# Performance work log

Hardware: AMD Instinct MI355X
Metric: run time of the kernel (lower is better)

## Reference

```python
import jax, jax.numpy as jnp
import numpy as np

B, T, E, H, HD = 4, 1500, 1280, 20, 64
SCALING = HD ** -0.5


def setup_inputs() -> dict:
    key = jax.random.key(0)
    ks = jax.random.split(key, 8)
    s = 0.02
    return {
        "hidden_states": jax.random.normal(ks[0], (B, 1, T, E), jnp.float32),
        "attention_mask": jnp.zeros((B, 1, T, T), jnp.float32),
        "Wq": jax.random.normal(ks[1], (H, HD, E), jnp.float32) * s,
        "bq": jax.random.normal(ks[2], (H, HD), jnp.float32) * s,
        "Wk": jax.random.normal(ks[3], (H, HD, E), jnp.float32) * s,
        "Wv": jax.random.normal(ks[4], (H, HD, E), jnp.float32) * s,
        "bv": jax.random.normal(ks[5], (H, HD), jnp.float32) * s,
        "Wo": jax.random.normal(ks[6], (E, E), jnp.float32) * s,
        "bo": jax.random.normal(ks[7], (E,), jnp.float32) * s,
    }


def reference(hidden_states, attention_mask, Wq, bq, Wk, Wv, bv, Wo, bo):
    # hidden_states: [B, 1, T, E] (NHWC with H=1, as in the torch module)
    b, _, t, e = hidden_states.shape
    x = hidden_states[:, 0]  # [B, T, E]
    # Per-head 1x1 Conv2d projections == batched linear over stacked head weights.
    # Scaling is folded into q (the module bakes it into q_proj weights/bias).
    q = (jnp.einsum("bte,hde->bhtd", x, Wq) + bq[None, :, None, :]) * SCALING
    k = jnp.einsum("bse,hde->bhsd", x, Wk)
    v = jnp.einsum("bse,hde->bhsd", x, Wv) + bv[None, :, None, :]
    # attention_mask broadcasts over the head dim (module adds it per head as [B,1,T,S])
    scores = jnp.einsum("bhtd,bhsd->bhts", q, k) + attention_mask  # [B,H,T,S]
    attn = jax.nn.softmax(scores, axis=-1)
    out = jnp.einsum("bhts,bhsd->bhtd", attn, v)  # [B,H,T,HD]
    out = out.transpose(0, 2, 1, 3).reshape(b, t, e)  # concat heads on channel dim
    final = jnp.einsum("bte,fe->btf", out, Wo) + bo  # 1x1 Conv2d out_proj
    return final[:, None, :, :]  # [B,1,T,E]
```

## Files before the change

kernel.cpp:

```cpp
#include <hip/hip_runtime.h>

#define T_LEN 1500
#define TP    1536
#define EDIM  1280
#define NH    20
#define HD    64
#define KDIM  1280
#define NT    20

#define LOG2E 1.4426950408889634f

#define OFF_X    ((size_t)0)
#define OFF_AO   ((size_t)0)
#define OFF_W    ((size_t)7700480)
#define OFF_WO   ((size_t)12615680)
#define OFF_Q    ((size_t)14254080)
#define OFF_K    ((size_t)22118400)
#define OFF_VT   ((size_t)29982720)

typedef float  f32x4  __attribute__((ext_vector_type(4)));
typedef float  f32x16 __attribute__((ext_vector_type(16)));
typedef short  s16x8  __attribute__((ext_vector_type(8)));
typedef __bf16 bf16x8 __attribute__((ext_vector_type(8)));
typedef unsigned short u16;
typedef unsigned int   u32;
typedef unsigned int u32x4 __attribute__((ext_vector_type(4)));

__device__ __forceinline__ f32x4 mfma_bf16(s16x8 a, s16x8 b, f32x4 c) {
  return __builtin_amdgcn_mfma_f32_16x16x32_bf16(
      __builtin_bit_cast(bf16x8, a), __builtin_bit_cast(bf16x8, b), c, 0, 0, 0);
}

__device__ __forceinline__ f32x16 mfma32(s16x8 a, s16x8 b, f32x16 c) {
  return __builtin_amdgcn_mfma_f32_32x32x16_bf16(
      __builtin_bit_cast(bf16x8, a), __builtin_bit_cast(bf16x8, b), c, 0, 0, 0);
}

__device__ __forceinline__ u16 f2bf(float f) {
  union { float f; unsigned int u; } a; a.f = f;
  return (u16)((a.u + 0x7fffu + ((a.u >> 16) & 1u)) >> 16);
}

__device__ __forceinline__ float fexp2(float x) {
  return __builtin_amdgcn_exp2f(x);
}

__device__ __forceinline__ void gl_lds16(const u16* g, u16* l) {
  __builtin_amdgcn_global_load_lds(
      (const __attribute__((address_space(1))) unsigned int*)(const void*)g,
      (__attribute__((address_space(3))) unsigned int*)(void*)l, 16, 0, 0);
}


__global__ __launch_bounds__(256) void prep_kernel(
    const float* __restrict__ x, const float* __restrict__ wq,
    const float* __restrict__ wk, const float* __restrict__ wv,
    const float* __restrict__ wo, const float* __restrict__ mask,
    u16* __restrict__ ws, u32* __restrict__ nzflags) {
  const int S0 = 1925120;
  const int S1 = 1228800;
  const int S2 = 409600;
  const int P1 = 46080;
  const int S3 = 2250000;
  const int TOT = S0 + S1 + S2 + 3 * P1 + S3;
  for (int v = blockIdx.x * 256 + threadIdx.x; v < TOT; v += gridDim.x * 256) {
    if (v < S0) {
      int i = v * 4;
      int m = i / EDIM, e = i - m * EDIM;
      int ep = (e & ~63) | (((((e >> 3) & 7) ^ (m & 7))) << 3) | (e & 7);
      ushort4 o;
      if (m < 6000) {
        float4 f = *(const float4*)(x + i);
        o = make_ushort4(f2bf(f.x), f2bf(f.y), f2bf(f.z), f2bf(f.w));
      } else {
        o = make_ushort4(0, 0, 0, 0);
      }
      *(ushort4*)(ws + OFF_X + (size_t)m * EDIM + ep) = o;
    } else if (v < S0 + S1) {
      int j = (v - S0) * 4;
      int n = j / EDIM, e = j - n * EDIM;
      const float* s = (n < 1280) ? wq + (size_t)n * EDIM + e
                     : (n < 2560) ? wk + (size_t)(n - 1280) * EDIM + e
                                  : wv + (size_t)(n - 2560) * EDIM + e;
      float4 f = *(const float4*)s;
      int ep = (e & ~63) | (((((e >> 3) & 7) ^ (n & 7))) << 3) | (e & 7);
      *(ushort4*)(ws + OFF_W + (size_t)n * EDIM + ep) =
          make_ushort4(f2bf(f.x), f2bf(f.y), f2bf(f.z), f2bf(f.w));
    } else if (v < S0 + S1 + S2) {
      int j = (v - S0 - S1) * 4;
      int n = j / EDIM, e = j - n * EDIM;
      float4 f = *(const float4*)(wo + j);
      int ep = (e & ~63) | (((((e >> 3) & 7) ^ (n & 7))) << 3) | (e & 7);
      *(ushort4*)(ws + OFF_WO + (size_t)n * EDIM + ep) =
          make_ushort4(f2bf(f.x), f2bf(f.y), f2bf(f.z), f2bf(f.w));
    } else if (v < S0 + S1 + S2 + 3 * P1) {
      int p = v - (S0 + S1 + S2);
      ushort4 z = make_ushort4(0, 0, 0, 0);
      if (p < P1) {
        int p4 = p * 4; int bh = p4 / 2304; int rem = p4 - bh * 2304;
        int tt = rem >> 6, d = rem & 63;
        *(ushort4*)(ws + OFF_Q + ((size_t)(bh * TP + 1500 + tt)) * HD + d) = z;
      } else if (p < 2 * P1) {
        int p4 = (p - P1) * 4; int bh = p4 / 2304; int rem = p4 - bh * 2304;
        int tt = rem >> 6, d = rem & 63;
        *(ushort4*)(ws + OFF_K + ((size_t)(bh * TP + 1500 + tt)) * HD + d) = z;
      } else {
        int p4 = (p - 2 * P1) * 4; int bh = p4 / 2304; int rem = p4 - bh * 2304;
        int d = rem / 36, ss = rem - d * 36;
        int t = 1500 + ss;
        int tphys = (t & ~63) | (((((t >> 3) & 7) ^ (d & 7))) << 3) | (t & 7);
        *(ushort4*)(ws + OFF_VT + ((size_t)(bh * HD + d)) * TP + tphys) = z;
      }
    } else {
      int p = v - (S0 + S1 + S2 + 3 * P1);
      int i4 = p * 4;
      int bb = i4 / 2250000;
      int rem = i4 - bb * 2250000;
      int q = rem / 1500;
      int s = rem - q * 1500;
      float4 f = *(const float4*)(mask + (size_t)bb * 2250000 + rem);
      if (f.x != 0.f || f.y != 0.f || f.z != 0.f || f.w != 0.f)
        atomicOr(&nzflags[(bb * 12 + (q >> 7)) * 24 + (s >> 6)], 1u);
    }
  }
}

__device__ __forceinline__ void gemm_mainloop256(
    const u16* __restrict__ A, const u16* __restrict__ B,
    int mt, int nt, u16* lds, f32x4 acc[4][4]) {
  const int tid = threadIdx.x;
  const int lane = tid & 63, wid = tid >> 6;
  const int lg = lane >> 4, lr = lane & 15;
  const int wr = wid >> 1, wn = wid & 1;

  const u16* aB = A + (size_t)(mt * 256) * KDIM;
  const u16* bB = B + (size_t)(nt * 128) * KDIM;
  size_t aOff[4], bOff[2];
  #pragma unroll
  for (int l = 0; l < 4; ++l) {
    int gid = l * 512 + tid;
    aOff[l] = (size_t)(gid >> 3) * KDIM + (gid & 7) * 8;
  }
  #pragma unroll
  for (int l = 0; l < 2; ++l) {
    int gid = l * 512 + tid;
    bOff[l] = (size_t)(gid >> 3) * KDIM + (gid & 7) * 8;
  }
  const int ldsOff = tid * 8;
  int arow[4], brow[4];
  #pragma unroll
  for (int i = 0; i < 4; ++i) arow[i] = (wr * 64 + i * 16 + lr) * 64;
  #pragma unroll
  for (int j = 0; j < 4; ++j) brow[j] = (wn * 64 + j * 16 + lr) * 64;
  const int gsw0 = ((lg) ^ (lr & 7)) * 8;
  const int gsw1 = ((4 + lg) ^ (lr & 7)) * 8;

  #pragma unroll
  for (int t = 0; t < 2; ++t) {
    u16* dA = lds + t * 24576;
    u16* dB = dA + 16384;
    #pragma unroll
    for (int l = 0; l < 4; ++l) gl_lds16(aB + aOff[l] + t * 64, dA + ldsOff + l * 4096);
    #pragma unroll
    for (int l = 0; l < 2; ++l) gl_lds16(bB + bOff[l] + t * 64, dB + ldsOff + l * 4096);
  }

  int s = 0;
  #pragma unroll 1
  for (int kt = 0; kt < NT; ++kt) {
    if (kt < NT - 1) asm volatile("s_waitcnt vmcnt(6)" ::: "memory");
    else             asm volatile("s_waitcnt vmcnt(0)" ::: "memory");
    __builtin_amdgcn_s_barrier();
    __builtin_amdgcn_sched_barrier(0);
    u16* cA = lds + s * 24576;
    u16* cB = cA + 16384;
    int ssl = s + 2; if (ssl >= 3) ssl -= 3;
    u16* sA = lds + ssl * 24576;
    u16* sB = sA + 16384;
    const bool doStage = (kt + 2 < NT);
    if (doStage) {
      gl_lds16(aB + aOff[0] + (kt + 2) * 64, sA + ldsOff);
      gl_lds16(aB + aOff[1] + (kt + 2) * 64, sA + ldsOff + 4096);
      gl_lds16(bB + bOff[0] + (kt + 2) * 64, sB + ldsOff);
    }
    {
      s16x8 af[4], bg[4];
      #pragma unroll
      for (int i = 0; i < 4; ++i) af[i] = *(const s16x8*)(cA + arow[i] + gsw0);
      #pragma unroll
      for (int j = 0; j < 4; ++j) bg[j] = *(const s16x8*)(cB + brow[j] + gsw0);
      __builtin_amdgcn_s_setprio(1);
      #pragma unroll
      for (int i = 0; i < 4; ++i)
        #pragma unroll
        for (int j = 0; j < 4; ++j)
          acc[i][j] = mfma_bf16(af[i], bg[j], acc[i][j]);
      __builtin_amdgcn_s_setprio(0);
    }
    __builtin_amdgcn_s_barrier();
    if (doStage) {
      gl_lds16(aB + aOff[2] + (kt + 2) * 64, sA + ldsOff + 8192);
      gl_lds16(aB + aOff[3] + (kt + 2) * 64, sA + ldsOff + 12288);
      gl_lds16(bB + bOff[1] + (kt + 2) * 64, sB + ldsOff + 4096);
    }
    {
      s16x8 af[4], bg[4];
      #pragma unroll
      for (int i = 0; i < 4; ++i) af[i] = *(const s16x8*)(cA + arow[i] + gsw1);
      #pragma unroll
      for (int j = 0; j < 4; ++j) bg[j] = *(const s16x8*)(cB + brow[j] + gsw1);
      __builtin_amdgcn_s_setprio(1);
      #pragma unroll
      for (int i = 0; i < 4; ++i)
        #pragma unroll
        for (int j = 0; j < 4; ++j)
          acc[i][j] = mfma_bf16(af[i], bg[j], acc[i][j]);
      __builtin_amdgcn_s_setprio(0);
    }
    s = s + 1; if (s >= 3) s = 0;
  }
}

__global__ __launch_bounds__(512) void gemm_qkv_kernel(
    const u16* __restrict__ X, const u16* __restrict__ W,
    const float* __restrict__ bq, const float* __restrict__ bv,
    u16* __restrict__ Qw, u16* __restrict__ Kw, u16* __restrict__ Vtw) {
  __shared__ __align__(16) u16 lds[3 * 24576];
  const int bid = blockIdx.x;
  const int xcd = bid & 7, idx = bid >> 3;
  const int mt = xcd * 3 + idx % 3;
  const int nt = idx / 3;
  f32x4 acc[4][4] = {};
  gemm_mainloop256(X, W, mt, nt, lds, acc);
  const int tid = threadIdx.x;
  const int lane = tid & 63, wid = tid >> 6;
  const int lg = lane >> 4, lr = lane & 15;
  const int wr = wid >> 1, wn = wid & 1;
  #pragma unroll
  for (int i = 0; i < 4; ++i) {
    #pragma unroll
    for (int r = 0; r < 4; ++r) {
      int mm = mt * 256 + wr * 64 + i * 16 + lg * 4 + r;
      if (mm >= 6000) continue;
      int bt = mm / 1500, tt = mm - bt * 1500;
      #pragma unroll
      for (int j = 0; j < 4; ++j) {
        int n = nt * 128 + wn * 64 + j * 16 + lr;
        float v = acc[i][j][r];
        if (n < 1280) {
          int hh = n >> 6, d = n & 63;
          Qw[((size_t)(bt * NH + hh) * TP + tt) * HD + d] =
              f2bf((v + bq[n]) * (0.125f * LOG2E));
        } else if (n < 2560) {
          int nn = n - 1280, hh = nn >> 6, d = nn & 63;
          int dp = ((((d >> 3) ^ (tt & 7))) << 3) | (d & 7);
          Kw[((size_t)(bt * NH + hh) * TP + tt) * HD + dp] = f2bf(v);
        } else {
          int nn = n - 2560, hh = nn >> 6, d = nn & 63;
          int tphys = (tt & ~63) | (((((tt >> 3) & 7) ^ (d & 7))) << 3) | (tt & 7);
          Vtw[((size_t)(bt * NH + hh) * HD + d) * TP + tphys] = f2bf(v + bv[nn]);
        }
      }
    }
  }
}

__global__ __launch_bounds__(256) void attn_kernel(
    const u16* __restrict__ Qw, const u16* __restrict__ Kw,
    const u16* __restrict__ Vtw, const float* __restrict__ mask,
    const u32* __restrict__ nzflags, u16* __restrict__ AO) {
  __shared__ __align__(16) u16 Kb[2][64 * 64];
  __shared__ __align__(16) u16 Vb[2][64 * 64];
  const int bhid = blockIdx.y;
  const int bb = bhid / NH, hh = bhid % NH;
  const int tid = threadIdx.x;
  const int w = tid >> 6;
  const int lane = tid & 63;
  const int lq = lane & 31;
  const int hi = lane >> 5;
  const int q0 = blockIdx.x * 128 + w * 32;
  const int qrow = q0 + lq;
  const int qm = qrow < (T_LEN - 1) ? qrow : (T_LEN - 1);
  const u16* Qp = Qw + (size_t)bhid * TP * HD;
  const u16* Kp = Kw + (size_t)bhid * TP * HD;
  const u16* Vp = Vtw + (size_t)bhid * HD * TP;
  const float* mp = mask + (size_t)bb * T_LEN * T_LEN + (size_t)qm * T_LEN;
  const u32* nzp = nzflags + (bb * 12 + blockIdx.x) * 24;

  s16x8 qf[4];
  #pragma unroll
  for (int c = 0; c < 4; ++c)
    qf[c] = *(const s16x8*)(Qp + (size_t)qrow * HD + c * 16 + hi * 8);

  f32x16 O0 = {}, O1 = {};
  float m = -3e38f, l = 0.f;

  {
    gl_lds16(Kp + tid * 8,                 Kb[0] + tid * 8);
    gl_lds16(Kp + 2048 + tid * 8,          Kb[0] + 2048 + tid * 8);
    int r = tid >> 3, g = tid & 7;
    gl_lds16(Vp + (size_t)r * TP + g * 8,          Vb[0] + tid * 8);
    gl_lds16(Vp + (size_t)(r + 32) * TP + g * 8,   Vb[0] + 2048 + tid * 8);
  }
  __syncthreads();

  int buf = 0;
  #pragma unroll 1
  for (int st = 0; st < 24; ++st) {
    const int s0 = st * 64;
    if (st < 23) {
      const int sn = s0 + 64;
      gl_lds16(Kp + (size_t)sn * HD + tid * 8,        Kb[buf ^ 1] + tid * 8);
      gl_lds16(Kp + (size_t)sn * HD + 2048 + tid * 8, Kb[buf ^ 1] + 2048 + tid * 8);
      int r = tid >> 3, g = tid & 7;
      gl_lds16(Vp + (size_t)r * TP + sn + g * 8,        Vb[buf ^ 1] + tid * 8);
      gl_lds16(Vp + (size_t)(r + 32) * TP + sn + g * 8, Vb[buf ^ 1] + 2048 + tid * 8);
    }
    const bool has_mask = nzp[st] != 0u;
    const u16* kb = Kb[buf];
    f32x16 S0a = {}, S1a = {};
    #pragma unroll
    for (int c = 0; c < 4; ++c) {
      int gc = 2 * c + hi;
      int gs = (gc ^ (lq & 7)) << 3;
      s16x8 k0 = *(const s16x8*)(kb + lq * 64 + gs);
      s16x8 k1 = *(const s16x8*)(kb + (32 + lq) * 64 + gs);
      S0a = mfma32(k0, qf[c], S0a);
      S1a = mfma32(k1, qf[c], S1a);
    }
    float p[32];
    #pragma unroll
    for (int r = 0; r < 16; ++r) { p[r] = S0a[r]; p[16 + r] = S1a[r]; }
    if (has_mask) {
      f32x4 mk[2][4];
      #pragma unroll
      for (int sh = 0; sh < 2; ++sh)
        #pragma unroll
        for (int g = 0; g < 4; ++g) {
          int sb = s0 + sh * 32 + 8 * g + 4 * hi;
          if (sb > T_LEN - 4) sb = T_LEN - 4;
          mk[sh][g] = *(const f32x4*)(mp + sb);
        }
      #pragma unroll
      for (int r = 0; r < 16; ++r) {
        p[r]      = fmaf(mk[0][r >> 2][r & 3], LOG2E, p[r]);
        p[16 + r] = fmaf(mk[1][r >> 2][r & 3], LOG2E, p[16 + r]);
      }
    }
    if (st == 23) {
      if (hi) { p[12] = p[13] = p[14] = p[15] = -1e30f; }
      #pragma unroll
      for (int r = 16; r < 32; ++r) p[r] = -1e30f;
    }
    float t1[16];
    #pragma unroll
    for (int r = 0; r < 16; ++r) t1[r] = fmaxf(p[r], p[r + 16]);
    #pragma unroll
    for (int r = 0; r < 8; ++r) t1[r] = fmaxf(t1[r], t1[r + 8]);
    float mx = fmaxf(fmaxf(fmaxf(t1[0], t1[1]), fmaxf(t1[2], t1[3])),
                     fmaxf(fmaxf(t1[4], t1[5]), fmaxf(t1[6], t1[7])));
    mx = fmaxf(mx, __shfl_xor(mx, 32));
    if (!__all(mx <= m + 8.f)) {
      float mn = fmaxf(m, mx);
      float sc = fexp2(m - mn);
      O0 *= sc; O1 *= sc; l *= sc;
      m = mn;
    }
    #pragma unroll
    for (int r = 0; r < 32; ++r) p[r] = fexp2(p[r] - m);
    float s1[16];
    #pragma unroll
    for (int r = 0; r < 16; ++r) s1[r] = p[r] + p[r + 16];
    #pragma unroll
    for (int r = 0; r < 8; ++r) s1[r] += s1[r + 8];
    #pragma unroll
    for (int r = 0; r < 4; ++r) s1[r] += s1[r + 4];
    float rs = (s1[0] + s1[1]) + (s1[2] + s1[3]);
    rs += __shfl_xor(rs, 32);
    l += rs;
    const u16* vb = Vb[buf];
    #pragma unroll
    for (int sh = 0; sh < 2; ++sh) {
      u32 pk[8];
      #pragma unroll
      for (int j = 0; j < 8; ++j)
        asm("v_cvt_pk_bf16_f32 %0, %1, %2"
            : "=v"(pk[j]) : "v"(p[sh * 16 + 2 * j]), "v"(p[sh * 16 + 2 * j + 1]));
      asm("v_permlane32_swap_b32 %0, %1" : "+v"(pk[0]), "+v"(pk[2]));
      asm("v_permlane32_swap_b32 %0, %1" : "+v"(pk[1]), "+v"(pk[3]));
      asm("v_permlane32_swap_b32 %0, %1" : "+v"(pk[4]), "+v"(pk[6]));
      asm("v_permlane32_swap_b32 %0, %1" : "+v"(pk[5]), "+v"(pk[7]));
      u32x4 ta = {pk[0], pk[1], pk[2], pk[3]};
      u32x4 tb = {pk[4], pk[5], pk[6], pk[7]};
      s16x8 pfa = __builtin_bit_cast(s16x8, ta);
      s16x8 pfb = __builtin_bit_cast(s16x8, tb);
      int ga = sh * 4 + hi, gb = sh * 4 + 2 + hi;
      {
        int d = lq;
        s16x8 va = *(const s16x8*)(vb + d * 64 + ((ga ^ (d & 7)) << 3));
        s16x8 vc = *(const s16x8*)(vb + d * 64 + ((gb ^ (d & 7)) << 3));
        O0 = mfma32(va, pfa, O0);
        O0 = mfma32(vc, pfb, O0);
      }
      {
        int d = 32 + lq;
        s16x8 va = *(const s16x8*)(vb + d * 64 + ((ga ^ (d & 7)) << 3));
        s16x8 vc = *(const s16x8*)(vb + d * 64 + ((gb ^ (d & 7)) << 3));
        O1 = mfma32(va, pfa, O1);
        O1 = mfma32(vc, pfb, O1);
      }
    }
    __syncthreads();
    buf ^= 1;
  }

  if (qrow < T_LEN) {
    float inv = 1.f / l;
    int arow = bb * T_LEN + qrow;
    int key = arow & 7;
    size_t base = (size_t)arow * EDIM + hh * 64;
    #pragma unroll
    for (int g = 0; g < 4; ++g) {
      ushort4 o0, o1;
      o0.x = f2bf(O0[4 * g + 0] * inv); o0.y = f2bf(O0[4 * g + 1] * inv);
      o0.z = f2bf(O0[4 * g + 2] * inv); o0.w = f2bf(O0[4 * g + 3] * inv);
      o1.x = f2bf(O1[4 * g + 0] * inv); o1.y = f2bf(O1[4 * g + 1] * inv);
      o1.z = f2bf(O1[4 * g + 2] * inv); o1.w = f2bf(O1[4 * g + 3] * inv);
      *(ushort4*)(AO + base + ((g ^ key) << 3) + 4 * hi)       = o0;
      *(ushort4*)(AO + base + (((4 + g) ^ key) << 3) + 4 * hi) = o1;
    }
  }
}

__global__ __launch_bounds__(512) void gemm_out_kernel(
    const u16* __restrict__ AOb, const u16* __restrict__ Wob,
    const float* __restrict__ bo, float* __restrict__ out) {
  __shared__ __align__(16) u16 lds[3 * 24576];
  const int bid = blockIdx.x;
  const int xcd = bid & 7, idx = bid >> 3;
  const int mt = xcd * 3 + idx % 3;
  const int nt = idx / 3;
  f32x4 acc[4][4] = {};
  gemm_mainloop256(AOb, Wob, mt, nt, lds, acc);
  const int tid = threadIdx.x;
  const int lane = tid & 63, wid = tid >> 6;
  const int lg = lane >> 4, lr = lane & 15;
  const int wr = wid >> 1, wn = wid & 1;
  #pragma unroll
  for (int i = 0; i < 4; ++i) {
    #pragma unroll
    for (int r = 0; r < 4; ++r) {
      int mm = mt * 256 + wr * 64 + i * 16 + lg * 4 + r;
      if (mm >= 6000) continue;
      #pragma unroll
      for (int j = 0; j < 4; ++j) {
        int n = nt * 128 + wn * 64 + j * 16 + lr;
        out[(size_t)mm * EDIM + n] = acc[i][j][r] + bo[n];
      }
    }
  }
}

extern "C" void kernel_launch(void* const* d_in, const int* in_sizes, int n_in,
                              void* d_out, int out_size, void* d_ws, size_t ws_size,
                              hipStream_t stream) {
  const float* x    = (const float*)d_in[0];
  const float* mask = (const float*)d_in[1];
  const float* wq   = (const float*)d_in[2];
  const float* bq   = (const float*)d_in[3];
  const float* wk   = (const float*)d_in[4];
  const float* wv   = (const float*)d_in[5];
  const float* bv   = (const float*)d_in[6];
  const float* wo   = (const float*)d_in[7];
  const float* bo   = (const float*)d_in[8];
  float* out = (float*)d_out;
  u16* ws = (u16*)d_ws;
  u32* nzflags = (u32*)d_out;

  hipMemsetAsync(nzflags, 0, 1152 * sizeof(u32), stream);
  prep_kernel<<<2048, 256, 0, stream>>>(x, wq, wk, wv, wo, mask, ws, nzflags);
  gemm_qkv_kernel<<<720, 512, 0, stream>>>(
      ws + OFF_X, ws + OFF_W, bq, bv, ws + OFF_Q, ws + OFF_K, ws + OFF_VT);
  attn_kernel<<<dim3(12, 80), 256, 0, stream>>>(
      ws + OFF_Q, ws + OFF_K, ws + OFF_VT, mask, nzflags, ws + OFF_AO);
  gemm_out_kernel<<<240, 512, 0, stream>>>(
      ws + OFF_AO, ws + OFF_WO, bo, out);
}
```

Measured before the change: 244.4 us.

## Software-pipeline LDS fragment loads across k-steps in QKV GEMM mainloop

Restructures the GEMM mainloop so each set of LDS fragment reads is issued before the MFMA block that consumes the previous set. The first half of the next tile is read just before the second-half MFMAs of the current tile, and one barrier per iteration is removed. This overlaps LDS read latency with matrix-core work. The cost is extra fragment registers live at once, which could raise register pressure, and the barrier and waitcnt ordering becomes more delicate.

New measurement: 245.9 us (median of 2 runs). No clear change (+0.6%).

```diff
diff --git a/kernel.cpp b/kernel.cpp
--- a/kernel.cpp
+++ b/kernel.cpp
@@ -159,19 +159,25 @@
   for (int t = 0; t < 2; ++t) {
     u16* dA = lds + t * 24576;
     u16* dB = dA + 16384;
-    #pragma unroll
-    for (int l = 0; l < 4; ++l) gl_lds16(aB + aOff[l] + t * 64, dA + ldsOff + l * 4096);
-    #pragma unroll
-    for (int l = 0; l < 2; ++l) gl_lds16(bB + bOff[l] + t * 64, dB + ldsOff + l * 4096);
-  }
+    gl_lds16(aB + aOff[0] + t * 64, dA + ldsOff);
+    gl_lds16(aB + aOff[1] + t * 64, dA + ldsOff + 4096);
+    gl_lds16(bB + bOff[0] + t * 64, dB + ldsOff);
+    gl_lds16(aB + aOff[2] + t * 64, dA + ldsOff + 8192);
+    gl_lds16(aB + aOff[3] + t * 64, dA + ldsOff + 12288);
+    gl_lds16(bB + bOff[1] + t * 64, dB + ldsOff + 4096);
+  }
+  asm volatile("s_waitcnt vmcnt(6)" ::: "memory");
+  __builtin_amdgcn_s_barrier();
+  __builtin_amdgcn_sched_barrier(0);
+  s16x8 ca[4], cb[4];
+  #pragma unroll
+  for (int i = 0; i < 4; ++i) ca[i] = *(const s16x8*)(lds + arow[i] + gsw0);
+  #pragma unroll
+  for (int j = 0; j < 4; ++j) cb[j] = *(const s16x8*)(lds + 16384 + brow[j] + gsw0);
 
   int s = 0;
   #pragma unroll 1
   for (int kt = 0; kt < NT; ++kt) {
-    if (kt < NT - 1) asm volatile("s_waitcnt vmcnt(6)" ::: "memory");
-    else             asm volatile("s_waitcnt vmcnt(0)" ::: "memory");
-    __builtin_amdgcn_s_barrier();
-    __builtin_amdgcn_sched_barrier(0);
     u16* cA = lds + s * 24576;
     u16* cB = cA + 16384;
     int ssl = s + 2; if (ssl >= 3) ssl -= 3;
@@ -183,40 +189,44 @@
       gl_lds16(aB + aOff[1] + (kt + 2) * 64, sA + ldsOff + 4096);
       gl_lds16(bB + bOff[0] + (kt + 2) * 64, sB + ldsOff);
     }
-    {
-      s16x8 af[4], bg[4];
-      #pragma unroll
-      for (int i = 0; i < 4; ++i) af[i] = *(const s16x8*)(cA + arow[i] + gsw0);
-      #pragma unroll
-      for (int j = 0; j < 4; ++j) bg[j] = *(const s16x8*)(cB + brow[j] + gsw0);
-      __builtin_amdgcn_s_setprio(1);
-      #pragma unroll
-      for (int i = 0; i < 4; ++i)
-        #pragma unroll
-        for (int j = 0; j < 4; ++j)
-          acc[i][j] = mfma_bf16(af[i], bg[j], acc[i][j]);
-      __builtin_amdgcn_s_setprio(0);
-    }
-    __builtin_amdgcn_s_barrier();
+    s16x8 na[4], nb[4];
+    #pragma unroll
+    for (int i = 0; i < 4; ++i) na[i] = *(const s16x8*)(cA + arow[i] + gsw1);
+    #pragma unroll
+    for (int j = 0; j < 4; ++j) nb[j] = *(const s16x8*)(cB + brow[j] + gsw1);
+    __builtin_amdgcn_s_setprio(1);
+    #pragma unroll
+    for (int i = 0; i < 4; ++i)
+      #pragma unroll
+      for (int j = 0; j < 4; ++j)
+        acc[i][j] = mfma_bf16(ca[i], cb[j], acc[i][j]);
+    __builtin_amdgcn_s_setprio(0);
     if (doStage) {
       gl_lds16(aB + aOff[2] + (kt + 2) * 64, sA + ldsOff + 8192);
       gl_lds16(aB + aOff[3] + (kt + 2) * 64, sA + ldsOff + 12288);
       gl_lds16(bB + bOff[1] + (kt + 2) * 64, sB + ldsOff + 4096);
     }
-    {
-      s16x8 af[4], bg[4];
-      #pragma unroll
-      for (int i = 0; i < 4; ++i) af[i] = *(const s16x8*)(cA + arow[i] + gsw1);
-      #pragma unroll
-      for (int j = 0; j < 4; ++j) bg[j] = *(const s16x8*)(cB + brow[j] + gsw1);
-      __builtin_amdgcn_s_setprio(1);
-      #pragma unroll
-      for (int i = 0; i < 4; ++i)
-        #pragma unroll
-        for (int j = 0; j < 4; ++j)
-          acc[i][j] = mfma_bf16(af[i], bg[j], acc[i][j]);
-      __builtin_amdgcn_s_setprio(0);
-    }
+    if (kt < NT - 1) {
+      asm volatile("s_waitcnt lgkmcnt(0)" ::: "memory");
+      if (kt < NT - 2) asm volatile("s_waitcnt vmcnt(6)" ::: "memory");
+      else             asm volatile("s_waitcnt vmcnt(0)" ::: "memory");
+      __builtin_amdgcn_s_barrier();
+      __builtin_amdgcn_sched_barrier(0);
+      int sn = s + 1; if (sn >= 3) sn = 0;
+      const u16* nA = lds + sn * 24576;
+      const u16* nB2 = nA + 16384;
+      #pragma unroll
+      for (int i = 0; i < 4; ++i) ca[i] = *(const s16x8*)(nA + arow[i] + gsw0);
+      #pragma unroll
+      for (int j = 0; j < 4; ++j) cb[j] = *(const s16x8*)(nB2 + brow[j] + gsw0);
+    }
+    __builtin_amdgcn_s_setprio(1);
+    #pragma unroll
+    for (int i = 0; i < 4; ++i)
+      #pragma unroll
+      for (int j = 0; j < 4; ++j)
+        acc[i][j] = mfma_bf16(na[i], nb[j], acc[i][j]);
+    __builtin_amdgcn_s_setprio(0);
     s = s + 1; if (s >= 3) s = 0;
   }
 }
```
